# Kernel optimization log

Measured on AMD Instinct MI355X. Metric: run time of the kernel, lower is better.

Reference implementation:

```python
import jax, jax.numpy as jnp
import numpy as np

N_SPK = 2048
M_UTT = 16
D_EMB = 512
EPS = 1e-8  # torch cosine_similarity eps


def setup_inputs() -> dict:
    key = jax.random.key(0)
    k1, = jax.random.split(key, 1)
    speaker_vectors = jax.random.normal(k1, (N_SPK * M_UTT, D_EMB), dtype=jnp.float32)
    return {
        "speaker_vectors": speaker_vectors,
        "w": jnp.float32(10.0),
        "b": jnp.float32(-5.0),
        "speakers": N_SPK,
    }


def _normalize(x):
    # torch.cosine_similarity clamps each norm at eps
    n = jnp.maximum(jnp.linalg.norm(x, axis=-1, keepdims=True), EPS)
    return x / n


def reference(speaker_vectors, w, b, speakers):
    N = speakers
    NM, D = speaker_vectors.shape
    M = NM // N
    v3 = speaker_vectors.reshape(N, M, D)
    ssum = v3.sum(axis=1)                         # [N, D] per-speaker sums
    C = ssum / M                                  # full centroids [N, D]
    C_min = (ssum[:, None, :] - v3) / (M - 1)     # leave-one-out centroids [N, M, D]

    vn = _normalize(speaker_vectors)              # [NM, D]
    # diagonal similarities: cos(C_min[j], v[j]) per utterance j
    S_diag = jnp.sum(_normalize(C_min.reshape(NM, D)) * vn, axis=-1)  # [NM]
    # full similarity matrix via one normalized matmul: [N, NM]
    S_full = _normalize(C) @ vn.T
    # replace each speaker's own block row entries with leave-one-out sims
    col_spk = jnp.arange(NM) // M                 # speaker id of each column
    same = col_spk[None, :] == jnp.arange(N)[:, None]  # [N, NM]
    S = jnp.where(same, S_diag[None, :], S_full)

    # L_j = -(w*S_diag_j + b) + log sum_n exp(w*S[n,j] + b)
    L = -(w * S_diag + b) + jax.nn.logsumexp(w * S + b, axis=0)
    return L.sum()
```

## Files before the change

kernel.cpp:

```cpp
#include <hip/hip_runtime.h>
#include <stdint.h>

#define N_SPK 2048
#define M_UTT 16
#define D_EMB 512
#define NM (N_SPK * M_UTT)
#define FP8_SCALE 16.0f

typedef __attribute__((ext_vector_type(4))) float f32x4;
typedef __attribute__((ext_vector_type(4))) int   i32x4;
typedef __attribute__((ext_vector_type(8))) int   i32x8;

__device__ __forceinline__ void async_copy16(const void* g, void* l) {
    __builtin_amdgcn_global_load_lds(
        (const __attribute__((address_space(1))) unsigned int*)g,
        (__attribute__((address_space(3))) unsigned int*)l,
        16, 0, 0);
}

__device__ __forceinline__ i32x8 ld_frag(const unsigned char* base, int s0) {
    i32x4 lo = *(const i32x4*)(base + s0 * 16);
    i32x4 hi = *(const i32x4*)(base + (s0 ^ 1) * 16);
    return __builtin_shufflevector(lo, hi, 0, 1, 2, 3, 4, 5, 6, 7);
}

__global__ __launch_bounds__(256) void prep_kernel(
    const float* __restrict__ V, const float* __restrict__ wp,
    const float* __restrict__ bp, unsigned char* __restrict__ Cn8,
    unsigned char* __restrict__ vn8, float* __restrict__ dterm,
    float* __restrict__ colsum, float* __restrict__ out)
{
    const int spk = blockIdx.x, t = threadIdx.x;
    const int wave = t >> 6, lane = t & 63;
    const float2* vb = (const float2*)(V + (size_t)spk * (M_UTT * D_EMB));

    __shared__ __align__(16) float red[32][264];
    __shared__ float red2[32];
    __shared__ float invs[M_UTT];
    __shared__ float wred[4];

    if (spk < 128) colsum[spk * 256 + t] = 0.f;
    if (spk == 0 && t == 0) out[0] = 0.f;

    float2 p[M_UTT];
#pragma unroll
    for (int m = 0; m < M_UTT; ++m) p[m] = vb[m * 256 + t];

    float2 ss = make_float2(0.f, 0.f);
#pragma unroll
    for (int m = 0; m < M_UTT; ++m) { ss.x += p[m].x; ss.y += p[m].y; }

    float cnp = ss.x * ss.x + ss.y * ss.y;
#pragma unroll
    for (int off = 32; off > 0; off >>= 1) cnp += __shfl_xor(cnp, off);
    if (lane == 0) wred[wave] = cnp;

#pragma unroll
    for (int m = 0; m < M_UTT; ++m) {
        red[m][t]         = ss.x * p[m].x + ss.y * p[m].y;
        red[m + M_UTT][t] = p[m].x * p[m].x + p[m].y * p[m].y;
    }
    __syncthreads();
    const float cn2 = wred[0] + wred[1] + wred[2] + wred[3];

    {
        const int r = t >> 3, s = t & 7;
        const float4* rp = (const float4*)red;
        float4 a = make_float4(0.f, 0.f, 0.f, 0.f);
#pragma unroll
        for (int k = 0; k < 8; ++k) {
            float4 q = rp[r * 66 + s + 8 * k];
            a.x += q.x; a.y += q.y; a.z += q.z; a.w += q.w;
        }
        float v1 = (a.x + a.y) + (a.z + a.w);
        v1 += __shfl_xor(v1, 1);
        v1 += __shfl_xor(v1, 2);
        v1 += __shfl_xor(v1, 4);
        if (s == 0) red2[r] = v1;
    }
    __syncthreads();

    if (t < M_UTT) {
        const float sv = red2[t], vv = red2[t + M_UTT];
        const float cc = cn2 - 2.f * sv + vv;
        const float cv = sv - vv;
        const float dc = fmaxf(sqrtf(fmaxf(cc, 0.f)) * (1.f / (M_UTT - 1)), 1e-8f) * (M_UTT - 1);
        const float dv = fmaxf(sqrtf(vv), 1e-8f);
        dterm[spk * M_UTT + t] = (*wp) * (cv / (dc * dv)) + (*bp);
        invs[t] = FP8_SCALE / dv;
    }
    __syncthreads();

    const float cs = FP8_SCALE / (M_UTT * fmaxf(sqrtf(cn2) * (1.f / M_UTT), 1e-8f));
    {
        int pk = __builtin_amdgcn_cvt_pk_fp8_f32(ss.x * cs, ss.y * cs, 0, false);
        ((unsigned short*)(Cn8 + (size_t)spk * D_EMB))[t] = (unsigned short)pk;
    }
#pragma unroll
    for (int m = 0; m < M_UTT; ++m) {
        const float iv = invs[m];
        int pk = __builtin_amdgcn_cvt_pk_fp8_f32(p[m].x * iv, p[m].y * iv, 0, false);
        ((unsigned short*)(vn8 + ((size_t)(spk * M_UTT + m)) * D_EMB))[t] = (unsigned short)pk;
    }
}

__global__ __launch_bounds__(256) void gemm_kernel(
    const unsigned char* __restrict__ Cn8, const unsigned char* __restrict__ vn8,
    const float* __restrict__ wp, const float* __restrict__ bp,
    float* __restrict__ colsum)
{
    __shared__ __align__(16) unsigned char As[128 * 256];
    __shared__ __align__(16) unsigned char Bs[128 * 256];
    __shared__ float csum[128];

    const int tid = threadIdx.x;
    const int w = tid >> 6, l = tid & 63;
    const int by = blockIdx.x;
    const int bx = blockIdx.y;
    const float wgt = (*wp) * (1.f / (FP8_SCALE * FP8_SCALE));
    const float bsc = *bp;

    if (tid < 128) csum[tid] = 0.f;

    const int r_l = l >> 4, hh = (l >> 3) & 1, sl8 = l & 7;
    const int g_even = sl8 ^ r_l;
    const size_t rowoff = (size_t)(w * 32 + r_l) * D_EMB + hh * 128;
    const unsigned char* Ab0 = Cn8 + (size_t)(by * 128) * D_EMB + rowoff + g_even * 16;
    const unsigned char* Ab1 = Cn8 + (size_t)(by * 128) * D_EMB + rowoff + (g_even ^ 4) * 16;
    const unsigned char* Bb0 = vn8 + (size_t)(bx * 128) * D_EMB + rowoff + g_even * 16;
    const unsigned char* Bb1 = vn8 + (size_t)(bx * 128) * D_EMB + rowoff + (g_even ^ 4) * 16;
    unsigned char* AsW = As + (w * 32) * 256;
    unsigned char* BsW = Bs + (w * 32) * 256;

    const int wm = w & 1, wn = w >> 1;
    const int l16 = l & 15, q = l >> 4;
    const int s0 = (2 * q) ^ (l & 7);
    const unsigned char* Ard = As + (wm * 64 + l16) * 256;
    const unsigned char* Brd = Bs + (wn * 64 + l16) * 256;

    f32x4 acc[4][4];
    const f32x4 z = {0.f, 0.f, 0.f, 0.f};
#pragma unroll
    for (int i = 0; i < 4; ++i)
#pragma unroll
        for (int j = 0; j < 4; ++j) acc[i][j] = z;

#pragma unroll
    for (int kk = 0; kk < D_EMB; kk += 256) {
        __syncthreads();
#pragma unroll
        for (int i = 0; i < 8; ++i) {
            const unsigned char* pa = ((i & 1) ? Ab1 : Ab0) + i * 2048 + kk;
            const unsigned char* pb = ((i & 1) ? Bb1 : Bb0) + i * 2048 + kk;
            async_copy16(pa, AsW + i * 1024);
            async_copy16(pb, BsW + i * 1024);
        }
        __syncthreads();
#pragma unroll
        for (int h2 = 0; h2 < 2; ++h2) {
            const int ho = h2 * 128;
            i32x8 bfr[4];
#pragma unroll
            for (int j = 0; j < 4; ++j) bfr[j] = ld_frag(Brd + j * 4096 + ho, s0);
#pragma unroll
            for (int i = 0; i < 4; ++i) {
                i32x8 af = ld_frag(Ard + i * 4096 + ho, s0);
#pragma unroll
                for (int j = 0; j < 4; ++j)
                    acc[i][j] = __builtin_amdgcn_mfma_scale_f32_16x16x128_f8f6f4(
                        af, bfr[j], acc[i][j], 0, 0, 0, 0x7F7F7F7F, 0, 0x7F7F7F7F);
            }
        }
    }

    const int rowg0 = by * 128 + wm * 64 + q * 4;
    const int colg0 = bx * 128 + wn * 64 + l16;
#pragma unroll
    for (int j = 0; j < 4; ++j) {
        const int colg = colg0 + j * 16;
        const int cspk = colg >> 4;
        float p = 0.f;
#pragma unroll
        for (int i = 0; i < 4; ++i) {
            const int rowg = rowg0 + i * 16;
#pragma unroll
            for (int r = 0; r < 4; ++r) {
                float e = __expf(wgt * acc[i][j][r] + bsc);
                p += (rowg + r == cspk) ? 0.f : e;
            }
        }
        p += __shfl_xor(p, 16);
        p += __shfl_xor(p, 32);
        if (q == 0) atomicAdd(&csum[wn * 64 + j * 16 + l16], p);
    }
    __syncthreads();
    if (tid < 128) atomicAdd(&colsum[bx * 128 + tid], csum[tid]);
}

__global__ __launch_bounds__(256) void finish_kernel(
    const float* __restrict__ dterm, const float* __restrict__ colsum,
    float* __restrict__ out)
{
    const int idx = blockIdx.x * 256 + threadIdx.x;
    const int stride = gridDim.x * 256;
    float local = 0.f;
    for (int j = idx; j < NM; j += stride) {
        float t = dterm[j];
        local += logf(colsum[j] + __expf(t)) - t;
    }
#pragma unroll
    for (int off = 32; off > 0; off >>= 1) local += __shfl_xor(local, off);
    __shared__ float wr[4];
    const int wave = threadIdx.x >> 6, lane = threadIdx.x & 63;
    if (lane == 0) wr[wave] = local;
    __syncthreads();
    if (threadIdx.x == 0) atomicAdd(out, wr[0] + wr[1] + wr[2] + wr[3]);
}

extern "C" void kernel_launch(void* const* d_in, const int* in_sizes, int n_in,
                              void* d_out, int out_size, void* d_ws, size_t ws_size,
                              hipStream_t stream) {
    const float* V  = (const float*)d_in[0];
    const float* wp = (const float*)d_in[1];
    const float* bp = (const float*)d_in[2];

    char* ws = (char*)d_ws;
    unsigned char* Cn8 = (unsigned char*)ws;
    unsigned char* vn8 = (unsigned char*)(ws + ((size_t)1 << 20));
    float* dterm  = (float*)(ws + ((size_t)17 << 20));
    float* colsum = dterm + NM;
    float* out    = (float*)d_out;

    prep_kernel<<<N_SPK, 256, 0, stream>>>(V, wp, bp, Cn8, vn8, dterm, colsum, out);
    gemm_kernel<<<dim3(N_SPK / 128, NM / 128), 256, 0, stream>>>(Cn8, vn8, wp, bp, colsum);
    finish_kernel<<<64, 256, 0, stream>>>(dterm, colsum, out);
}
```

Baseline: 150.7 us.

## Double-buffer K tiles in fp8 GEMM and remap blocks for XCD locality

The GEMM kernel now loads 128-byte K slices into two LDS buffers and prefetches the next slice while MFMAs run on the current one, replacing the load-then-compute pattern over two 256-byte slices. It also remaps the linear block index so that consecutive blocks dispatched to the same XCD share B tiles, which should improve L2 reuse. The cost is an extra barrier per K step. There is also a correctness risk: the next-buffer writes are issued without waiting for the async loads to land before that buffer is read.

```diff
diff --git a/kernel.cpp b/kernel.cpp
--- a/kernel.cpp
+++ b/kernel.cpp
@@ -109,34 +109,31 @@
     const float* __restrict__ wp, const float* __restrict__ bp,
     float* __restrict__ colsum)
 {
-    __shared__ __align__(16) unsigned char As[128 * 256];
-    __shared__ __align__(16) unsigned char Bs[128 * 256];
+    __shared__ __align__(16) unsigned char As[2 * 128 * 128];
+    __shared__ __align__(16) unsigned char Bs[2 * 128 * 128];
     __shared__ float csum[128];
 
     const int tid = threadIdx.x;
     const int w = tid >> 6, l = tid & 63;
-    const int by = blockIdx.x;
-    const int bx = blockIdx.y;
+
+    const int p_lin = blockIdx.x + 16 * blockIdx.y;
+    const int L_log = (p_lin & 7) * 512 + (p_lin >> 3);
+    const int by = L_log & 15;
+    const int bx = L_log >> 4;
+
     const float wgt = (*wp) * (1.f / (FP8_SCALE * FP8_SCALE));
     const float bsc = *bp;
 
     if (tid < 128) csum[tid] = 0.f;
 
-    const int r_l = l >> 4, hh = (l >> 3) & 1, sl8 = l & 7;
-    const int g_even = sl8 ^ r_l;
-    const size_t rowoff = (size_t)(w * 32 + r_l) * D_EMB + hh * 128;
-    const unsigned char* Ab0 = Cn8 + (size_t)(by * 128) * D_EMB + rowoff + g_even * 16;
-    const unsigned char* Ab1 = Cn8 + (size_t)(by * 128) * D_EMB + rowoff + (g_even ^ 4) * 16;
-    const unsigned char* Bb0 = vn8 + (size_t)(bx * 128) * D_EMB + rowoff + g_even * 16;
-    const unsigned char* Bb1 = vn8 + (size_t)(bx * 128) * D_EMB + rowoff + (g_even ^ 4) * 16;
-    unsigned char* AsW = As + (w * 32) * 256;
-    unsigned char* BsW = Bs + (w * 32) * 256;
+    const int r_l = l >> 3, sl8 = l & 7;
+    const int g = sl8 ^ r_l;
+    const unsigned char* Ab = Cn8 + (size_t)(by * 128 + w * 32 + r_l) * D_EMB + g * 16;
+    const unsigned char* Bb = vn8 + (size_t)(bx * 128 + w * 32 + r_l) * D_EMB + g * 16;
 
     const int wm = w & 1, wn = w >> 1;
     const int l16 = l & 15, q = l >> 4;
     const int s0 = (2 * q) ^ (l & 7);
-    const unsigned char* Ard = As + (wm * 64 + l16) * 256;
-    const unsigned char* Brd = Bs + (wn * 64 + l16) * 256;
 
     f32x4 acc[4][4];
     const f32x4 z = {0.f, 0.f, 0.f, 0.f};
@@ -145,32 +142,44 @@
 #pragma unroll
         for (int j = 0; j < 4; ++j) acc[i][j] = z;
 
-#pragma unroll
-    for (int kk = 0; kk < D_EMB; kk += 256) {
+    {
+        unsigned char* AsW = As + (w * 32) * 128;
+        unsigned char* BsW = Bs + (w * 32) * 128;
+#pragma unroll
+        for (int i = 0; i < 4; ++i) {
+            async_copy16(Ab + i * 4096, AsW + i * 1024);
+            async_copy16(Bb + i * 4096, BsW + i * 1024);
+        }
+    }
+    __syncthreads();
+
+#pragma unroll
+    for (int t = 0; t < 4; ++t) {
+        const int buf = t & 1;
+        if (t + 1 < 4) {
+            const int kk = (t + 1) * 128;
+            unsigned char* AsW = As + (buf ^ 1) * 16384 + (w * 32) * 128;
+            unsigned char* BsW = Bs + (buf ^ 1) * 16384 + (w * 32) * 128;
+#pragma unroll
+            for (int i = 0; i < 4; ++i) {
+                async_copy16(Ab + i * 4096 + kk, AsW + i * 1024);
+                async_copy16(Bb + i * 4096 + kk, BsW + i * 1024);
+            }
+        }
+        const unsigned char* Ard = As + buf * 16384 + (wm * 64 + l16) * 128;
+        const unsigned char* Brd = Bs + buf * 16384 + (wn * 64 + l16) * 128;
+        i32x8 bfr[4];
+#pragma unroll
+        for (int j = 0; j < 4; ++j) bfr[j] = ld_frag(Brd + j * 2048, s0);
+#pragma unroll
+        for (int i = 0; i < 4; ++i) {
+            i32x8 af = ld_frag(Ard + i * 2048, s0);
+#pragma unroll
+            for (int j = 0; j < 4; ++j)
+                acc[i][j] = __builtin_amdgcn_mfma_scale_f32_16x16x128_f8f6f4(
+                    af, bfr[j], acc[i][j], 0, 0, 0, 0x7F7F7F7F, 0, 0x7F7F7F7F);
+        }
         __syncthreads();
-#pragma unroll
-        for (int i = 0; i < 8; ++i) {
-            const unsigned char* pa = ((i & 1) ? Ab1 : Ab0) + i * 2048 + kk;
-            const unsigned char* pb = ((i & 1) ? Bb1 : Bb0) + i * 2048 + kk;
-            async_copy16(pa, AsW + i * 1024);
-            async_copy16(pb, BsW + i * 1024);
-        }
-        __syncthreads();
-#pragma unroll
-        for (int h2 = 0; h2 < 2; ++h2) {
-            const int ho = h2 * 128;
-            i32x8 bfr[4];
-#pragma unroll
-            for (int j = 0; j < 4; ++j) bfr[j] = ld_frag(Brd + j * 4096 + ho, s0);
-#pragma unroll
-            for (int i = 0; i < 4; ++i) {
-                i32x8 af = ld_frag(Ard + i * 4096 + ho, s0);
-#pragma unroll
-                for (int j = 0; j < 4; ++j)
-                    acc[i][j] = __builtin_amdgcn_mfma_scale_f32_16x16x128_f8f6f4(
-                        af, bfr[j], acc[i][j], 0, 0, 0, 0x7F7F7F7F, 0, 0x7F7F7F7F);
-            }
-        }
     }
 
     const int rowg0 = by * 128 + wm * 64 + q * 4;
```

After: 153.5 us. No clear change (+1.8%).
